# Optimization experiments

Measured on AMD Instinct MI355X. Metric: run time of the kernel, lower is better.

The kernel has to match this reference:

```python
import jax, jax.numpy as jnp
import numpy as np

B, Q, S, D, H = 8, 100, 4096, 256, 8
HD = D // H
EPS = 1e-5


def layer_norm(x, g, b):
    mu = jnp.mean(x, axis=-1, keepdims=True)
    var = jnp.mean(jnp.square(x - mu), axis=-1, keepdims=True)
    return (x - mu) * jax.lax.rsqrt(var + EPS) * g + b


def mha(q_in, k_in, v_in, w_in, b_in, w_out, b_out, bias=None):
    # torch nn.MultiheadAttention math (batch_first, dropout=0)
    wq, wk, wv = jnp.split(w_in, 3, axis=0)
    bq, bk, bv = jnp.split(b_in, 3, axis=0)
    Bq, Lq, _ = q_in.shape
    Lk = k_in.shape[1]
    q = (q_in @ wq.T + bq).reshape(Bq, Lq, H, HD)
    k = (k_in @ wk.T + bk).reshape(Bq, Lk, H, HD)
    v = (v_in @ wv.T + bv).reshape(Bq, Lk, H, HD)
    scores = jnp.einsum('bqhd,bkhd->bhqk', q, k) / jnp.sqrt(jnp.asarray(HD, q.dtype))
    if bias is not None:
        scores = scores + bias  # [B,1,Q,S] broadcast over heads (same per head)
    attn = jax.nn.softmax(scores, axis=-1)
    out = jnp.einsum('bhqk,bkhd->bqhd', attn, v).reshape(Bq, Lq, D)
    return out @ w_out.T + b_out


def setup_inputs() -> dict:
    key = jax.random.key(0)
    ks = jax.random.split(key, 12)
    s = 0.02
    return {
        'queries': jax.random.normal(ks[0], (B, Q, D), jnp.float32),
        'pixel_feat': jax.random.normal(ks[1], (B, S, D), jnp.float32),
        'prev_mask': jax.random.normal(ks[2], (B, Q, S), jnp.float32),
        'cross_in_w': jax.random.normal(ks[3], (3 * D, D), jnp.float32) * s,
        'cross_in_b': jnp.zeros((3 * D,), jnp.float32),
        'cross_out_w': jax.random.normal(ks[4], (D, D), jnp.float32) * s,
        'cross_out_b': jnp.zeros((D,), jnp.float32),
        'self_in_w': jax.random.normal(ks[5], (3 * D, D), jnp.float32) * s,
        'self_in_b': jnp.zeros((3 * D,), jnp.float32),
        'self_out_w': jax.random.normal(ks[6], (D, D), jnp.float32) * s,
        'self_out_b': jnp.zeros((D,), jnp.float32),
        'ln_cross_g': jnp.ones((D,), jnp.float32),
        'ln_cross_b': jnp.zeros((D,), jnp.float32),
        'ln_self_g': jnp.ones((D,), jnp.float32),
        'ln_self_b': jnp.zeros((D,), jnp.float32),
        'ln_ffn_g': jnp.ones((D,), jnp.float32),
        'ln_ffn_b': jnp.zeros((D,), jnp.float32),
        'ffn_w1': jax.random.normal(ks[7], (4 * D, D), jnp.float32) * s,
        'ffn_b1': jnp.zeros((4 * D,), jnp.float32),
        'ffn_w2': jax.random.normal(ks[8], (D, 4 * D), jnp.float32) * s,
        'ffn_b2': jnp.zeros((D,), jnp.float32),
    }


def reference(queries, pixel_feat, prev_mask,
              cross_in_w, cross_in_b, cross_out_w, cross_out_b,
              self_in_w, self_in_b, self_out_w, self_out_b,
              ln_cross_g, ln_cross_b, ln_self_g, ln_self_b, ln_ffn_g, ln_ffn_b,
              ffn_w1, ffn_b1, ffn_w2, ffn_b2):
    # masked cross-attn bias (no-grad region in torch; boolean ops have no grad)
    region = jax.nn.sigmoid(prev_mask) > 0.5                    # [B,Q,S]
    any_pos = jnp.any(region, axis=-1, keepdims=True)
    region = jnp.where(any_pos, region, jnp.ones_like(region))
    bias = (~region).astype(queries.dtype) * -10000.0
    bias = bias[:, None, :, :]                                  # [B,1,Q,S]

    q_out = mha(layer_norm(queries, ln_cross_g, ln_cross_b), pixel_feat, pixel_feat,
                cross_in_w, cross_in_b, cross_out_w, cross_out_b, bias)
    queries = queries + q_out

    q_norm = layer_norm(queries, ln_self_g, ln_self_b)
    q_out = mha(q_norm, q_norm, q_norm, self_in_w, self_in_b, self_out_w, self_out_b)
    queries = queries + q_out

    h = layer_norm(queries, ln_ffn_g, ln_ffn_b)
    h = jax.nn.gelu(h @ ffn_w1.T + ffn_b1, approximate=False) @ ffn_w2.T + ffn_b2
    return queries + h
```

## Files before the change

### kernel.cpp

```cpp
#include <hip/hip_runtime.h>
#include <hip/hip_bf16.h>
#include <math.h>

#define BQ 100
#define SB 8
#define SS 4096
#define DD 256
#define HH 8
#define HDD 32
#define NSPLIT 4
#define SCHUNK (SS / NSPLIT)
#define MROWS 800

typedef __attribute__((ext_vector_type(8))) short bf16x8;
typedef __attribute__((ext_vector_type(4))) float f32x4;

__device__ inline unsigned short f2bf(float f) {
    union { float f; unsigned u; } v; v.f = f;
    unsigned r = v.u + 0x7fff + ((v.u >> 16) & 1);
    return (unsigned short)(r >> 16);
}

__device__ inline unsigned pkbf(float x, float y) {
    union { __hip_bfloat162 h; unsigned u; } c;
    c.h = __float22bfloat162_rn(make_float2(x, y));
    return c.u;
}

__device__ inline bf16x8 load_bf8(const float* p) {
    float4 a = *(const float4*)p;
    float4 b = *(const float4*)(p + 4);
    union { unsigned u[4]; bf16x8 v; } r;
    r.u[0] = pkbf(a.x, a.y); r.u[1] = pkbf(a.z, a.w);
    r.u[2] = pkbf(b.x, b.y); r.u[3] = pkbf(b.z, b.w);
    return r.v;
}

typedef __attribute__((address_space(1))) const void gas_void;
typedef __attribute__((address_space(3))) void las_void;
__device__ inline void gl_lds16(const unsigned short* g, unsigned short* l) {
    __builtin_amdgcn_global_load_lds((gas_void*)g, (las_void*)l, 16, 0, 0);
}

#define TM 128
#define TN 128

#define WOFF_CW   0
#define WOFF_SIW  196608
#define WOFF_COW  393216
#define WOFF_SOW  458752
#define WOFF_F1   524288
#define WOFF_F2   786432
#define WTOT      1048576

__global__ __launch_bounds__(256) void wprep(
        const float* __restrict__ cw, const float* __restrict__ siw,
        const float* __restrict__ cow, const float* __restrict__ sow,
        const float* __restrict__ f1, const float* __restrict__ f2,
        const float* __restrict__ pix,
        unsigned short* __restrict__ o, unsigned short* __restrict__ abf) {
    int b = blockIdx.x;
    int t = threadIdx.x;
    if (b >= 512) {
        size_t off = (size_t)(b - 512) * 2048 + (size_t)t * 8;
        const float* p = pix + off;
        float4 a = *(const float4*)p;
        float4 c = *(const float4*)(p + 4);
        uint4 pk;
        pk.x = pkbf(a.x, a.y); pk.y = pkbf(a.z, a.w);
        pk.z = pkbf(c.x, c.y); pk.w = pkbf(c.z, c.w);
        *(uint4*)(abf + off) = pk;
        return;
    }
    const float* src; size_t so, doff;
    if (b < 96)       { src = cw;  so = (size_t)b * 2048;         doff = WOFF_CW; }
    else if (b < 192) { src = siw; so = (size_t)(b - 96) * 2048;  doff = WOFF_SIW; }
    else if (b < 224) { src = cow; so = (size_t)(b - 192) * 2048; doff = WOFF_COW; }
    else if (b < 256) { src = sow; so = (size_t)(b - 224) * 2048; doff = WOFF_SOW; }
    else if (b < 384) { src = f1;  so = (size_t)(b - 256) * 2048; doff = WOFF_F1; }
    else              { src = f2;  so = (size_t)(b - 384) * 2048; doff = WOFF_F2; }
    const float* p = src + so + (size_t)t * 8;
    float4 a = *(const float4*)p;
    float4 c = *(const float4*)(p + 4);
    uint4 pk;
    pk.x = pkbf(a.x, a.y); pk.y = pkbf(a.z, a.w);
    pk.z = pkbf(c.x, c.y); pk.w = pkbf(c.z, c.w);
    *(uint4*)(o + doff + so + (size_t)t * 8) = pk;
}

__global__ __launch_bounds__(256, 3) void stage1(
        const float* __restrict__ queries,
        const float* __restrict__ ln_g, const float* __restrict__ ln_b,
        const unsigned short* __restrict__ wbf,
        const float* __restrict__ cb,
        float* __restrict__ q_cross,
        const unsigned short* __restrict__ Abf,
        unsigned short* __restrict__ Kb, unsigned short* __restrict__ Vb,
        const float* __restrict__ mask, unsigned* __restrict__ Mbits) {
    __shared__ __align__(16) char smem[32768];
    const int bid = blockIdx.x;
    const int t = threadIdx.x;

    if (bid < 1024) {
        unsigned short* As = (unsigned short*)smem;
        unsigned short* Bs = As + 128 * 64;
        const unsigned short* Wb = wbf + (size_t)DD * DD;
        const float* bias = cb + DD;
        int xcd = bid & 7, idx = bid >> 3;
        int mt = xcd + 8 * (idx >> 2);
        int ntl = idx & 3;
        int m0 = mt * TM, n0 = ntl * TN;
        int wave = t >> 6, lane = t & 63;
        int wm = (wave & 1) * 64, wn = (wave >> 1) * 64;
        int fr = lane & 15, quad = lane >> 4;
        f32x4 acc[4][4] = {};

        int crow[4], ccol[4];
#pragma unroll
        for (int i = 0; i < 4; i++) {
            int c = i * 256 + t;
            crow[i] = c >> 3;
            ccol[i] = (c & 7) ^ (crow[i] & 7);
        }

        for (int k0 = 0; k0 < DD; k0 += 64) {
            __syncthreads();
#pragma unroll
            for (int i = 0; i < 4; i++) {
                gl_lds16(Abf + (size_t)(m0 + crow[i]) * DD + k0 + ccol[i] * 8,
                         As + (i * 256 + t) * 8);
                gl_lds16(Wb + (size_t)(n0 + crow[i]) * DD + k0 + ccol[i] * 8,
                         Bs + (i * 256 + t) * 8);
            }
            __syncthreads();
#pragma unroll
            for (int kk = 0; kk < 2; kk++) {
                bf16x8 af[4], bv[4];
#pragma unroll
                for (int mi = 0; mi < 4; mi++) {
                    int row = wm + mi * 16 + fr;
                    int j = (kk * 4 + quad) ^ (row & 7);
                    af[mi] = *(const bf16x8*)(As + row * 64 + j * 8);
                }
#pragma unroll
                for (int ni = 0; ni < 4; ni++) {
                    int row = wn + ni * 16 + fr;
                    int j = (kk * 4 + quad) ^ (row & 7);
                    bv[ni] = *(const bf16x8*)(Bs + row * 64 + j * 8);
                }
#pragma unroll
                for (int mi = 0; mi < 4; mi++) {
                    acc[mi][0] = __builtin_amdgcn_mfma_f32_16x16x32_bf16(af[mi], bv[0], acc[mi][0], 0, 0, 0);
                    acc[mi][1] = __builtin_amdgcn_mfma_f32_16x16x32_bf16(af[mi], bv[1], acc[mi][1], 0, 0, 0);
                    acc[mi][2] = __builtin_amdgcn_mfma_f32_16x16x32_bf16(af[mi], bv[2], acc[mi][2], 0, 0, 0);
                    acc[mi][3] = __builtin_amdgcn_mfma_f32_16x16x32_bf16(af[mi], bv[3], acc[mi][3], 0, 0, 0);
                }
            }
        }
#pragma unroll
        for (int ni = 0; ni < 4; ni++) {
            int n = n0 + wn + ni * 16 + fr;
            float bv = bias[n];
            unsigned short* dst = (n < 256) ? Kb : Vb;
            int hh = (n >> 5) & 7, d = n & 31;
#pragma unroll
            for (int mi = 0; mi < 4; mi++) {
#pragma unroll
                for (int r = 0; r < 4; r++) {
                    int m = m0 + wm + mi * 16 + quad * 4 + r;
                    int bb = m >> 12, s = m & (SS - 1);
                    dst[((((size_t)bb * HH + hh) * SS + s) << 5) + d] =
                        f2bf(acc[mi][ni][r] + bv);
                }
            }
        }
    } else if (bid < 1824) {
        int row = bid - 1024;
        unsigned* words = (unsigned*)smem;
        unsigned* orred = (unsigned*)(smem + 512);
        int w = t >> 6, lane = t & 63;
        const float* mp = mask + (size_t)row * SS + lane;
        float mv[16];
#pragma unroll
        for (int i = 0; i < 16; i++) mv[i] = mp[(w * 16 + i) * 64];
        unsigned lor = 0;
#pragma unroll
        for (int i = 0; i < 16; i++) {
            unsigned long long bal = __ballot(mv[i] > 0.f);
            if (lane == 0) {
                words[(w * 16 + i) * 2] = (unsigned)bal;
                words[(w * 16 + i) * 2 + 1] = (unsigned)(bal >> 32);
            }
            lor |= (unsigned)(bal | (bal >> 32));
        }
        if (lane == 0) orred[w] = lor;
        __syncthreads();
        unsigned anyv = orred[0] | orred[1] | orred[2] | orred[3];
        if (t < 128) Mbits[(size_t)row * 128 + t] = anyv ? words[t] : 0xFFFFFFFFu;
    } else {
        typedef unsigned short (*arow_t)[264];
        arow_t Aq = (arow_t)smem;
        float* mu_s = (float*)(smem + 16896);
        float* rs_s = mu_s + 32;
        float (*prt)[8][2] = (float(*)[8][2])(rs_s + 32);
        int idx = bid - 1824;
        int nq = idx & 1, my = idx >> 1;
        int m0 = my * 32;
        int row = t & 31, cs = t >> 5;
        const float* xp = queries + (size_t)(m0 + row) * DD + cs * 32;
        float s = 0.f, ss = 0.f;
#pragma unroll
        for (int c = 0; c < 32; c += 4) {
            float4 v = *(const float4*)(xp + c);
            s += v.x + v.y + v.z + v.w;
            ss += v.x * v.x + v.y * v.y + v.z * v.z + v.w * v.w;
        }
        prt[row][cs][0] = s; prt[row][cs][1] = ss;
        __syncthreads();
        if (t < 32) {
            float sum = 0.f, sq = 0.f;
#pragma unroll
            for (int k = 0; k < 8; k++) { sum += prt[t][k][0]; sq += prt[t][k][1]; }
            float mu = sum * (1.0f / DD);
            float var = sq * (1.0f / DD) - mu * mu;
            mu_s[t] = mu;
            rs_s[t] = rsqrtf(var + 1e-5f);
        }
        __syncthreads();
        {
            float mu = mu_s[row], r = rs_s[row];
            int col0 = cs * 32;
#pragma unroll
            for (int c = 0; c < 32; c += 8) {
                int col = col0 + c;
                float4 v0 = *(const float4*)(xp + c);
                float4 v1 = *(const float4*)(xp + c + 4);
                float4 g0 = *(const float4*)(ln_g + col);
                float4 g1 = *(const float4*)(ln_g + col + 4);
                float4 b0 = *(const float4*)(ln_b + col);
                float4 b1 = *(const float4*)(ln_b + col + 4);
                uint4 pk;
                pk.x = pkbf((v0.x - mu) * r * g0.x + b0.x, (v0.y - mu) * r * g0.y + b0.y);
                pk.y = pkbf((v0.z - mu) * r * g0.z + b0.z, (v0.w - mu) * r * g0.w + b0.w);
                pk.z = pkbf((v1.x - mu) * r * g1.x + b1.x, (v1.y - mu) * r * g1.y + b1.y);
                pk.w = pkbf((v1.z - mu) * r * g1.z + b1.z, (v1.w - mu) * r * g1.w + b1.w);
                *(uint4*)&Aq[row][col] = pk;
            }
        }
        __syncthreads();
        int w = t >> 6, lane = t & 63;
        int fr = lane & 15, quad = lane >> 4;
        int n0 = nq * 128 + w * 32;
        f32x4 acc[2][2] = {};
        const unsigned short* Wq0 = wbf + (size_t)(n0 + fr) * DD + quad * 8;
        const unsigned short* Wq1 = Wq0 + (size_t)16 * DD;
#pragma unroll
        for (int k0 = 0; k0 < DD; k0 += 32) {
            bf16x8 a0 = *(const bf16x8*)&Aq[fr][k0 + quad * 8];
            bf16x8 a1 = *(const bf16x8*)&Aq[16 + fr][k0 + quad * 8];
            bf16x8 w0 = *(const bf16x8*)(Wq0 + k0);
            bf16x8 w1 = *(const bf16x8*)(Wq1 + k0);
            acc[0][0] = __builtin_amdgcn_mfma_f32_16x16x32_bf16(a0, w0, acc[0][0], 0, 0, 0);
            acc[0][1] = __builtin_amdgcn_mfma_f32_16x16x32_bf16(a0, w1, acc[0][1], 0, 0, 0);
            acc[1][0] = __builtin_amdgcn_mfma_f32_16x16x32_bf16(a1, w0, acc[1][0], 0, 0, 0);
            acc[1][1] = __builtin_amdgcn_mfma_f32_16x16x32_bf16(a1, w1, acc[1][1], 0, 0, 0);
        }
#pragma unroll
        for (int ni = 0; ni < 2; ni++) {
            int n = n0 + ni * 16 + fr;
            float bv = cb[n];
#pragma unroll
            for (int mi = 0; mi < 2; mi++) {
#pragma unroll
                for (int r = 0; r < 4; r++) {
                    int m = m0 + mi * 16 + quad * 4 + r;
                    q_cross[(size_t)m * DD + n] = acc[mi][ni][r] + bv;
                }
            }
        }
    }
}

template<int MODE>
__global__ __launch_bounds__(64, 4) void ln_gemm(
        const float* __restrict__ X, const float* __restrict__ gam,
        const float* __restrict__ bet,
        const unsigned short* __restrict__ W, const float* __restrict__ bias,
        const float* __restrict__ res,
        float* __restrict__ C, int N) {
    __shared__ unsigned short As[32][264];
    __shared__ float mu_s[32], rs_s[32];
    __shared__ float prt[32][2][2];
    const int t = threadIdx.x;
    const int fr = t & 15, quad = t >> 4;
    const int m0 = blockIdx.y * 32, n0 = blockIdx.x * 32;
    const int row = t & 31, half = t >> 5;

    const float* xp = X + (size_t)(m0 + row) * DD + half * 128;
    float s = 0.f, ss = 0.f;
#pragma unroll
    for (int c = 0; c < 128; c += 4) {
        float4 v = *(const float4*)(xp + c);
        s += v.x + v.y + v.z + v.w;
        ss += v.x * v.x + v.y * v.y + v.z * v.z + v.w * v.w;
    }
    prt[row][half][0] = s;
    prt[row][half][1] = ss;
    __syncthreads();
    if (t < 32) {
        float sum = prt[t][0][0] + prt[t][1][0];
        float sq  = prt[t][0][1] + prt[t][1][1];
        float mu = sum * (1.0f / DD);
        float var = sq * (1.0f / DD) - mu * mu;
        mu_s[t] = mu;
        rs_s[t] = rsqrtf(var + 1e-5f);
    }
    __syncthreads();
    {
        float mu = mu_s[row], r = rs_s[row];
#pragma unroll
        for (int c = 0; c < 128; c += 8) {
            int col = half * 128 + c;
            float4 v0 = *(const float4*)(xp + c);
            float4 v1 = *(const float4*)(xp + c + 4);
            float4 g0 = *(const float4*)(gam + col);
            float4 g1 = *(const float4*)(gam + col + 4);
            float4 b0 = *(const float4*)(bet + col);
            float4 b1 = *(const float4*)(bet + col + 4);
            uint4 pk;
            pk.x = pkbf((v0.x - mu) * r * g0.x + b0.x, (v0.y - mu) * r * g0.y + b0.y);
            pk.y = pkbf((v0.z - mu) * r * g0.z + b0.z, (v0.w - mu) * r * g0.w + b0.w);
            pk.z = pkbf((v1.x - mu) * r * g1.x + b1.x, (v1.y - mu) * r * g1.y + b1.y);
            pk.w = pkbf((v1.z - mu) * r * g1.z + b1.z, (v1.w - mu) * r * g1.w + b1.w);
            *(uint4*)&As[row][col] = pk;
        }
    }
    __syncthreads();

    f32x4 acc[2][2] = {};
    const unsigned short* Wp0 = W + (size_t)(n0 + fr) * DD + quad * 8;
    const unsigned short* Wp1 = Wp0 + (size_t)16 * DD;
#pragma unroll
    for (int k0 = 0; k0 < DD; k0 += 32) {
        bf16x8 a0 = *(const bf16x8*)&As[fr][k0 + quad * 8];
        bf16x8 a1 = *(const bf16x8*)&As[16 + fr][k0 + quad * 8];
        bf16x8 w0 = *(const bf16x8*)(Wp0 + k0);
        bf16x8 w1 = *(const bf16x8*)(Wp1 + k0);
        acc[0][0] = __builtin_amdgcn_mfma_f32_16x16x32_bf16(a0, w0, acc[0][0], 0, 0, 0);
        acc[0][1] = __builtin_amdgcn_mfma_f32_16x16x32_bf16(a0, w1, acc[0][1], 0, 0, 0);
        acc[1][0] = __builtin_amdgcn_mfma_f32_16x16x32_bf16(a1, w0, acc[1][0], 0, 0, 0);
        acc[1][1] = __builtin_amdgcn_mfma_f32_16x16x32_bf16(a1, w1, acc[1][1], 0, 0, 0);
    }

#pragma unroll
    for (int ni = 0; ni < 2; ni++) {
        int n = n0 + ni * 16 + fr;
        float bv = bias[n];
#pragma unroll
        for (int mi = 0; mi < 2; mi++) {
#pragma unroll
            for (int r = 0; r < 4; r++) {
                int m = m0 + mi * 16 + quad * 4 + r;
                float v = acc[mi][ni][r] + bv;
                if (MODE == 1) {
                    v = 0.5f * v * (1.0f + erff(v * 0.70710678118654752f));
                } else if (MODE == 2) {
                    v += res[(size_t)m * N + n];
                }
                C[(size_t)m * N + n] = v;
            }
        }
    }
}

__global__ __launch_bounds__(64, 4) void comb_gemm(
        const float* __restrict__ Opart, const float* __restrict__ mpart,
        const float* __restrict__ lpart,
        const unsigned short* __restrict__ W, const float* __restrict__ bias,
        const float* __restrict__ res,
        float* __restrict__ C) {
    __shared__ unsigned short As[32][264];
    const int t = threadIdx.x;
    const int fr = t & 15, quad = t >> 4;
    const int m0 = blockIdx.y * 32, n0 = blockIdx.x * 32;
    const int row = t & 31, half = t >> 5;

    {
        int m = m0 + row;
        int b = m / BQ, q = m % BQ;
#pragma unroll
        for (int h = half * 4; h < half * 4 + 4; h++) {
            float mv[NSPLIT], wsp[NSPLIT];
            float mstar = -1e30f;
#pragma unroll
            for (int sp = 0; sp < NSPLIT; sp++) {
                mv[sp] = mpart[((size_t)(b * NSPLIT + sp) * HH + h) * BQ + q];
                mstar = fmaxf(mstar, mv[sp]);
            }
            float lstar = 0.f;
#pragma unroll
            for (int sp = 0; sp < NSPLIT; sp++) {
                wsp[sp] = __expf(mv[sp] - mstar);
                lstar += lpart[((size_t)(b * NSPLIT + sp) * HH + h) * BQ + q] * wsp[sp];
            }
            float inv = 1.0f / lstar;
#pragma unroll
            for (int d = 0; d < HDD; d += 8) {
                float o[8] = {};
#pragma unroll
                for (int sp = 0; sp < NSPLIT; sp++) {
                    const float* op = Opart +
                        ((size_t)(b * NSPLIT + sp) * BQ + q) * DD + h * HDD + d;
                    float4 a = *(const float4*)op;
                    float4 b4 = *(const float4*)(op + 4);
                    o[0] += a.x * wsp[sp];  o[1] += a.y * wsp[sp];
                    o[2] += a.z * wsp[sp];  o[3] += a.w * wsp[sp];
                    o[4] += b4.x * wsp[sp]; o[5] += b4.y * wsp[sp];
                    o[6] += b4.z * wsp[sp]; o[7] += b4.w * wsp[sp];
                }
                uint4 pk;
                pk.x = pkbf(o[0] * inv, o[1] * inv);
                pk.y = pkbf(o[2] * inv, o[3] * inv);
                pk.z = pkbf(o[4] * inv, o[5] * inv);
                pk.w = pkbf(o[6] * inv, o[7] * inv);
                *(uint4*)&As[row][h * HDD + d] = pk;
            }
        }
    }
    __syncthreads();

    f32x4 acc[2][2] = {};
    const unsigned short* Wp0 = W + (size_t)(n0 + fr) * DD + quad * 8;
    const unsigned short* Wp1 = Wp0 + (size_t)16 * DD;
#pragma unroll
    for (int k0 = 0; k0 < DD; k0 += 32) {
        bf16x8 a0 = *(const bf16x8*)&As[fr][k0 + quad * 8];
        bf16x8 a1 = *(const bf16x8*)&As[16 + fr][k0 + quad * 8];
        bf16x8 w0 = *(const bf16x8*)(Wp0 + k0);
        bf16x8 w1 = *(const bf16x8*)(Wp1 + k0);
        acc[0][0] = __builtin_amdgcn_mfma_f32_16x16x32_bf16(a0, w0, acc[0][0], 0, 0, 0);
        acc[0][1] = __builtin_amdgcn_mfma_f32_16x16x32_bf16(a0, w1, acc[0][1], 0, 0, 0);
        acc[1][0] = __builtin_amdgcn_mfma_f32_16x16x32_bf16(a1, w0, acc[1][0], 0, 0, 0);
        acc[1][1] = __builtin_amdgcn_mfma_f32_16x16x32_bf16(a1, w1, acc[1][1], 0, 0, 0);
    }

#pragma unroll
    for (int ni = 0; ni < 2; ni++) {
        int n = n0 + ni * 16 + fr;
        float bv = bias[n];
#pragma unroll
        for (int mi = 0; mi < 2; mi++) {
#pragma unroll
            for (int r = 0; r < 4; r++) {
                int m = m0 + mi * 16 + quad * 4 + r;
                float v = acc[mi][ni][r] + bv + res[(size_t)m * DD + n];
                C[(size_t)m * DD + n] = v;
            }
        }
    }
}

template<int KK, int SPLITK, int MODE>
__global__ __launch_bounds__(64, 4) void gemm_skinny2(
        const float* __restrict__ A, const unsigned short* __restrict__ W,
        const float* __restrict__ bias, const float* __restrict__ res,
        float* __restrict__ C, float* __restrict__ Cp, int N) {
    const int lane = threadIdx.x;
    const int fr = lane & 15, quad = lane >> 4;
    const int m0 = blockIdx.y * 32;
    const int n0 = blockIdx.x * 32;
    const int sk = blockIdx.z;
    const int KCH = KK / SPLITK;

    f32x4 acc[2][2] = {};
    const float* Ap0 = A + (size_t)(m0 + fr) * KK + sk * KCH + quad * 8;
    const float* Ap1 = Ap0 + (size_t)16 * KK;
    const unsigned short* Wp0 = W + (size_t)(n0 + fr) * KK + sk * KCH + quad * 8;
    const unsigned short* Wp1 = Wp0 + (size_t)16 * KK;

#pragma unroll
    for (int k0 = 0; k0 < KCH; k0 += 32) {
        bf16x8 a0 = load_bf8(Ap0 + k0);
        bf16x8 a1 = load_bf8(Ap1 + k0);
        bf16x8 w0 = *(const bf16x8*)(Wp0 + k0);
        bf16x8 w1 = *(const bf16x8*)(Wp1 + k0);
        acc[0][0] = __builtin_amdgcn_mfma_f32_16x16x32_bf16(a0, w0, acc[0][0], 0, 0, 0);
        acc[0][1] = __builtin_amdgcn_mfma_f32_16x16x32_bf16(a0, w1, acc[0][1], 0, 0, 0);
        acc[1][0] = __builtin_amdgcn_mfma_f32_16x16x32_bf16(a1, w0, acc[1][0], 0, 0, 0);
        acc[1][1] = __builtin_amdgcn_mfma_f32_16x16x32_bf16(a1, w1, acc[1][1], 0, 0, 0);
    }

    if (SPLITK == 1) {
#pragma unroll
        for (int ni = 0; ni < 2; ni++) {
            int n = n0 + ni * 16 + fr;
            float bv = bias[n];
#pragma unroll
            for (int mi = 0; mi < 2; mi++) {
#pragma unroll
                for (int r = 0; r < 4; r++) {
                    int m = m0 + mi * 16 + quad * 4 + r;
                    float v = acc[mi][ni][r] + bv;
                    if (MODE == 1) {
                        v = 0.5f * v * (1.0f + erff(v * 0.70710678118654752f));
                    } else if (MODE == 2) {
                        v += res[(size_t)m * N + n];
                    }
                    C[(size_t)m * N + n] = v;
                }
            }
        }
    } else {
        float* dst = Cp + (size_t)sk * MROWS * N;
#pragma unroll
        for (int ni = 0; ni < 2; ni++) {
            int n = n0 + ni * 16 + fr;
#pragma unroll
            for (int mi = 0; mi < 2; mi++) {
#pragma unroll
                for (int r = 0; r < 4; r++) {
                    int m = m0 + mi * 16 + quad * 4 + r;
                    dst[(size_t)m * N + n] = acc[mi][ni][r];
                }
            }
        }
    }
}

template<int SPLITK, int MODE>
__global__ void gemm_combine(const float* __restrict__ Cp,
                             const float* __restrict__ bias,
                             const float* __restrict__ res,
                             float* __restrict__ C, int N) {
    int m = blockIdx.x;
    for (int n = threadIdx.x; n < N; n += 256) {
        float v = bias[n];
#pragma unroll
        for (int sk = 0; sk < SPLITK; sk++)
            v += Cp[((size_t)sk * MROWS + m) * N + n];
        if (MODE == 1) {
            v = 0.5f * v * (1.0f + erff(v * 0.70710678118654752f));
        } else if (MODE == 2) {
            v += res[(size_t)m * N + n];
        }
        C[(size_t)m * N + n] = v;
    }
}

#define QT 64
#define ST 128

__global__ __launch_bounds__(256) void cross_attn_mfma(
        const float* __restrict__ Qm,
        const unsigned short* __restrict__ Kb,
        const unsigned short* __restrict__ Vb,
        const unsigned* __restrict__ Mbits,
        float* __restrict__ Opart,
        float* __restrict__ mpart,
        float* __restrict__ lpart) {
    __shared__ unsigned short Qs[QT][40];
    __shared__ unsigned short Ks[ST][40];
    __shared__ unsigned short Vt[HDD][136];
    __shared__ unsigned short Ps[QT][136];
    __shared__ unsigned Mq[QT][4];
    __shared__ float red[QT][17];
    __shared__ float m_s[QT], alpha_s[QT], l_s[QT];

    const int qb = blockIdx.x, h = blockIdx.y;
    const int b = blockIdx.z / NSPLIT, sp = blockIdx.z % NSPLIT;
    const int t = threadIdx.x;
    const int w = t >> 6, lane = t & 63;
    const int fr = lane & 15, quad = lane >> 4;
    const int q0 = qb * QT;
    const int qlim = min(BQ - q0, QT);

    {
        int q = t >> 2, c0 = (t & 3) * 8;
        float4 v0 = make_float4(0.f, 0.f, 0.f, 0.f), v1 = v0;
        if (q < qlim) {
            const float* qp = Qm + (size_t)(b * BQ + q0 + q) * DD + h * HDD + c0;
            v0 = *(const float4*)qp;
            v1 = *(const float4*)(qp + 4);
        }
        const float sc = 0.17677669529663687f;
        uint4 pq;
        pq.x = pkbf(v0.x * sc, v0.y * sc);
        pq.y = pkbf(v0.z * sc, v0.w * sc);
        pq.z = pkbf(v1.x * sc, v1.y * sc);
        pq.w = pkbf(v1.z * sc, v1.w * sc);
        *(uint4*)&Qs[q][c0] = pq;
        if (t < QT) { m_s[t] = -1e30f; l_s[t] = 0.f; }
    }

    f32x4 oacc[2] = {};
    const unsigned short* Kbase = Kb + (((size_t)(b * HH + h)) * SS << 5);
    const unsigned short* Vbase = Vb + (((size_t)(b * HH + h)) * SS << 5);

    for (int s0 = sp * SCHUNK; s0 < (sp + 1) * SCHUNK; s0 += ST) {
        __syncthreads();
        {
            int r = t >> 1, half = t & 1;
            const unsigned short* kp = Kbase + ((size_t)(s0 + r) << 5) + half * 16;
            *(uint4*)&Ks[r][half * 16] = *(const uint4*)kp;
            *(uint4*)&Ks[r][half * 16 + 8] = *(const uint4*)(kp + 8);
            const unsigned short* vp = Vbase + ((size_t)(s0 + r) << 5) + half * 16;
            union { uint4 u; unsigned short s[8]; } v0, v1;
            v0.u = *(const uint4*)vp;
            v1.u = *(const uint4*)(vp + 8);
#pragma unroll
            for (int j = 0; j < 8; j++) Vt[half * 16 + j][r] = v0.s[j];
#pragma unroll
            for (int j = 0; j < 8; j++) Vt[half * 16 + 8 + j][r] = v1.s[j];
        }
        {
            int q = t >> 2, wd = t & 3;
            unsigned mword = 0xFFFFFFFFu;
            if (q < qlim)
                mword = Mbits[(size_t)(b * BQ + q0 + q) * 128 + (s0 >> 5) + wd];
            Mq[q][wd] = mword;
        }
        __syncthreads();

        bf16x8 af[2];
#pragma unroll
        for (int mt = 0; mt < 2; mt++)
            af[mt] = *(const bf16x8*)&Ks[w * 32 + mt * 16 + fr][quad * 8];
        f32x4 st[2][4];
#pragma unroll
        for (int nt = 0; nt < 4; nt++) {
            bf16x8 bq = *(const bf16x8*)&Qs[nt * 16 + fr][quad * 8];
#pragma unroll
            for (int mt = 0; mt < 2; mt++) {
                f32x4 z = {0.f, 0.f, 0.f, 0.f};
                st[mt][nt] = __builtin_amdgcn_mfma_f32_16x16x32_bf16(af[mt], bq, z, 0, 0, 0);
            }
        }

        float pmax[4] = {-1e30f, -1e30f, -1e30f, -1e30f};
#pragma unroll
        for (int nt = 0; nt < 4; nt++) {
            unsigned mword = Mq[nt * 16 + fr][w];
#pragma unroll
            for (int mt = 0; mt < 2; mt++)
#pragma unroll
                for (int r = 0; r < 4; r++) {
                    int bitpos = mt * 16 + quad * 4 + r;
                    float v = st[mt][nt][r];
                    if (!((mword >> bitpos) & 1u)) v -= 10000.f;
                    st[mt][nt][r] = v;
                    pmax[nt] = fmaxf(pmax[nt], v);
                }
        }
#pragma unroll
        for (int nt = 0; nt < 4; nt++)
            red[nt * 16 + fr][w * 4 + quad] = pmax[nt];
        __syncthreads();

        if (t < QT) {
            float mt_ = -1e30f;
#pragma unroll
            for (int k = 0; k < 16; k++) mt_ = fmaxf(mt_, red[t][k]);
            float mo = m_s[t], mn = fmaxf(mo, mt_);
            m_s[t] = mn;
            alpha_s[t] = __expf(mo - mn);
        }
        __syncthreads();

        float psum[4] = {0.f, 0.f, 0.f, 0.f};
#pragma unroll
        for (int nt = 0; nt < 4; nt++) {
            float mrow = m_s[nt * 16 + fr];
#pragma unroll
            for (int mt = 0; mt < 2; mt++) {
                float p0 = __expf(st[mt][nt][0] - mrow);
                float p1 = __expf(st[mt][nt][1] - mrow);
                float p2 = __expf(st[mt][nt][2] - mrow);
                float p3 = __expf(st[mt][nt][3] - mrow);
                psum[nt] += p0 + p1 + p2 + p3;
                uint2 pk;
                pk.x = pkbf(p0, p1);
                pk.y = pkbf(p2, p3);
                *(uint2*)&Ps[nt * 16 + fr][w * 32 + mt * 16 + quad * 4] = pk;
            }
        }
#pragma unroll
        for (int nt = 0; nt < 4; nt++)
            red[nt * 16 + fr][w * 4 + quad] = psum[nt];
        __syncthreads();

        if (t < QT) {
            float s = 0.f;
#pragma unroll
            for (int k = 0; k < 16; k++) s += red[t][k];
            l_s[t] = l_s[t] * alpha_s[t] + s;
        }

#pragma unroll
        for (int r = 0; r < 4; r++) {
            float a = alpha_s[w * 16 + quad * 4 + r];
            oacc[0][r] *= a; oacc[1][r] *= a;
        }
#pragma unroll
        for (int k0 = 0; k0 < ST; k0 += 32) {
            bf16x8 ap = *(const bf16x8*)&Ps[w * 16 + fr][k0 + quad * 8];
            bf16x8 bv0 = *(const bf16x8*)&Vt[fr][k0 + quad * 8];
            bf16x8 bv1 = *(const bf16x8*)&Vt[16 + fr][k0 + quad * 8];
            oacc[0] = __builtin_amdgcn_mfma_f32_16x16x32_bf16(ap, bv0, oacc[0], 0, 0, 0);
            oacc[1] = __builtin_amdgcn_mfma_f32_16x16x32_bf16(ap, bv1, oacc[1], 0, 0, 0);
        }
    }
    __syncthreads();

    int part = b * NSPLIT + sp;
    if (t < qlim) {
        mpart[((size_t)part * HH + h) * BQ + q0 + t] = m_s[t];
        lpart[((size_t)part * HH + h) * BQ + q0 + t] = l_s[t];
    }
#pragma unroll
    for (int nd = 0; nd < 2; nd++) {
#pragma unroll
        for (int r = 0; r < 4; r++) {
            int q = w * 16 + quad * 4 + r;
            if (q < qlim)
                Opart[((size_t)part * BQ + q0 + q) * DD + h * HDD + nd * 16 + fr] = oacc[nd][r];
        }
    }
}

__global__ void attn_kernel(const float* __restrict__ Qm, int sq, int qo0,
                            const float* __restrict__ Km, int sk, int ko0,
                            const float* __restrict__ Vm, int sv, int vo0,
                            float* __restrict__ Out, int so, int oo0,
                            int Slen, int Qlen, float scale) {
    int q = blockIdx.x, h = blockIdx.y, b = blockIdx.z;
    int tid = threadIdx.x;
    __shared__ float qv[32];
    __shared__ float sc[128];
    __shared__ float red[256];
    __shared__ float part[8][33];
    int qrow = b * Qlen + q;
    if (tid < 32) qv[tid] = Qm[(size_t)qrow * sq + qo0 + h * HDD + tid] * scale;
    __syncthreads();

    float lmax = -1e30f;
    for (int s = tid; s < Slen; s += 256) {
        const float* kp = Km + (size_t)(b * Slen + s) * sk + ko0 + h * HDD;
        float dot = 0.f;
#pragma unroll
        for (int d = 0; d < HDD; d += 4) {
            float4 k4 = *(const float4*)(kp + d);
            dot += qv[d] * k4.x + qv[d + 1] * k4.y + qv[d + 2] * k4.z + qv[d + 3] * k4.w;
        }
        sc[s] = dot;
        lmax = fmaxf(lmax, dot);
    }
    red[tid] = lmax; __syncthreads();
    for (int off = 128; off > 0; off >>= 1) {
        if (tid < off) red[tid] = fmaxf(red[tid], red[tid + off]);
        __syncthreads();
    }
    float m = red[0];
    __syncthreads();
    float lsum = 0.f;
    for (int s = tid; s < Slen; s += 256) {
        float e = __expf(sc[s] - m);
        sc[s] = e;
        lsum += e;
    }
    red[tid] = lsum; __syncthreads();
    for (int off = 128; off > 0; off >>= 1) {
        if (tid < off) red[tid] += red[tid + off];
        __syncthreads();
    }
    float inv = 1.0f / red[0];

    int d = tid & 31, g = tid >> 5;
    float acc = 0.f;
    for (int s = g; s < Slen; s += 8)
        acc += sc[s] * Vm[(size_t)(b * Slen + s) * sv + vo0 + h * HDD + d];
    part[g][d] = acc; __syncthreads();
    if (g == 0) {
        float t = 0.f;
#pragma unroll
        for (int gg = 0; gg < 8; gg++) t += part[gg][d];
        Out[(size_t)qrow * so + oo0 + h * HDD + d] = t * inv;
    }
}

extern "C" void kernel_launch(void* const* d_in, const int* in_sizes, int n_in,
                              void* d_out, int out_size, void* d_ws, size_t ws_size,
                              hipStream_t stream) {
    const float* queries    = (const float*)d_in[0];
    const float* pixel_feat = (const float*)d_in[1];
    const float* prev_mask  = (const float*)d_in[2];
    const float* cross_in_w  = (const float*)d_in[3];
    const float* cross_in_b  = (const float*)d_in[4];
    const float* cross_out_w = (const float*)d_in[5];
    const float* cross_out_b = (const float*)d_in[6];
    const float* self_in_w   = (const float*)d_in[7];
    const float* self_in_b   = (const float*)d_in[8];
    const float* self_out_w  = (const float*)d_in[9];
    const float* self_out_b  = (const float*)d_in[10];
    const float* ln_cross_g  = (const float*)d_in[11];
    const float* ln_cross_b  = (const float*)d_in[12];
    const float* ln_self_g   = (const float*)d_in[13];
    const float* ln_self_b   = (const float*)d_in[14];
    const float* ln_ffn_g    = (const float*)d_in[15];
    const float* ln_ffn_b    = (const float*)d_in[16];
    const float* ffn_w1 = (const float*)d_in[17];
    const float* ffn_b1 = (const float*)d_in[18];
    const float* ffn_w2 = (const float*)d_in[19];
    const float* ffn_b2 = (const float*)d_in[20];
    float* out = (float*)d_out;

    const int NQ = SB * BQ;
    const int NK = SB * SS;

    float* ws = (float*)d_ws;
    unsigned* Mbits = (unsigned*)ws;   ws += (size_t)NQ * 128;
    float* q_cross  = ws;              ws += (size_t)NQ * DD;
    unsigned short* Kbk = (unsigned short*)ws;
    ws += (size_t)NK * DD / 2;
    unsigned short* Vbk = (unsigned short*)ws;
    ws += (size_t)NK * DD / 2;
    float* queries1 = ws;              ws += (size_t)NQ * DD;
    float* qkv      = ws;              ws += (size_t)NQ * 3 * DD;
    float* attn2    = ws;              ws += (size_t)NQ * DD;
    float* queries2 = ws;              ws += (size_t)NQ * DD;
    float* ffn_h    = ws;              ws += (size_t)NQ * 4 * DD;
    float* Csplit   = ws;              ws += (size_t)4 * MROWS * DD;
    float* Opart    = ws;              ws += (size_t)SB * NSPLIT * BQ * DD;
    float* mpart    = ws;              ws += (size_t)SB * NSPLIT * HH * BQ;
    float* lpart    = ws;              ws += (size_t)SB * NSPLIT * HH * BQ;
    unsigned short* wbf = (unsigned short*)ws;
    ws += WTOT / 2;
    unsigned short* Abf = (unsigned short*)ws;

    const float scale = 0.17677669529663687f;

    wprep<<<4608, 256, 0, stream>>>(
        cross_in_w, self_in_w, cross_out_w, self_out_w, ffn_w1, ffn_w2,
        pixel_feat, wbf, Abf);

    stage1<<<1874, 256, 0, stream>>>(
        queries, ln_cross_g, ln_cross_b, wbf, cross_in_b, q_cross,
        Abf, Kbk, Vbk, prev_mask, Mbits);

    cross_attn_mfma<<<dim3(2, HH, SB * NSPLIT), 256, 0, stream>>>(
        q_cross, Kbk, Vbk, Mbits, Opart, mpart, lpart);
    comb_gemm<<<dim3(8, 25), 64, 0, stream>>>(
        Opart, mpart, lpart, wbf + WOFF_COW, cross_out_b, queries, queries1);

    ln_gemm<0><<<dim3(24, 25), 64, 0, stream>>>(
        queries1, ln_self_g, ln_self_b, wbf + WOFF_SIW, self_in_b, nullptr,
        qkv, 3 * DD);
    attn_kernel<<<dim3(BQ, HH, SB), 256, 0, stream>>>(
        qkv, 3 * DD, 0, qkv, 3 * DD, DD, qkv, 3 * DD, 2 * DD,
        attn2, DD, 0, BQ, BQ, scale);
    gemm_skinny2<256, 1, 2><<<dim3(8, 25), 64, 0, stream>>>(
        attn2, wbf + WOFF_SOW, self_out_b, queries1, queries2, nullptr, DD);

    ln_gemm<1><<<dim3(32, 25), 64, 0, stream>>>(
        queries2, ln_ffn_g, ln_ffn_b, wbf + WOFF_F1, ffn_b1, nullptr,
        ffn_h, 4 * DD);
    gemm_skinny2<1024, 4, 2><<<dim3(8, 25, 4), 64, 0, stream>>>(
        ffn_h, wbf + WOFF_F2, ffn_b2, nullptr, nullptr, Csplit, DD);
    gemm_combine<4, 2><<<MROWS, 256, 0, stream>>>(
        Csplit, ffn_b2, queries2, out, DD);
}
```

Measured before the change: 253.9 us.

## Double-buffer K/V projection GEMM and replace scalar self-attention with MFMA kernel

The K/V projection GEMM in stage1 now uses a 32-wide K step with two LDS buffers. The next tile's loads are issued before computing on the current one, so a single barrier per step replaces the previous load/compute barrier pair. Separately, the per-query scalar self-attention kernel (800 blocks) is replaced by one block per (head, batch) that computes scores, softmax and P·V with bf16 MFMA. This drops scalar FP32 dot products and many small reductions, but lowers self-attention precision to bf16 and uses far fewer blocks.

```diff
diff --git a/kernel.cpp b/kernel.cpp
--- a/kernel.cpp
+++ b/kernel.cpp
@@ -102,60 +102,63 @@
     const int t = threadIdx.x;
 
     if (bid < 1024) {
-        unsigned short* As = (unsigned short*)smem;
-        unsigned short* Bs = As + 128 * 64;
+        unsigned short* Sbuf = (unsigned short*)smem;
         const unsigned short* Wb = wbf + (size_t)DD * DD;
         const float* bias = cb + DD;
         int xcd = bid & 7, idx = bid >> 3;
-        int mt = xcd + 8 * (idx >> 2);
+        int mtile = xcd + 8 * (idx >> 2);
         int ntl = idx & 3;
-        int m0 = mt * TM, n0 = ntl * TN;
+        int m0 = mtile * TM, n0 = ntl * TN;
         int wave = t >> 6, lane = t & 63;
         int wm = (wave & 1) * 64, wn = (wave >> 1) * 64;
         int fr = lane & 15, quad = lane >> 4;
         f32x4 acc[4][4] = {};
 
-        int crow[4], ccol[4];
-#pragma unroll
-        for (int i = 0; i < 4; i++) {
-            int c = i * 256 + t;
-            crow[i] = c >> 3;
-            ccol[i] = (c & 7) ^ (crow[i] & 7);
-        }
-
-        for (int k0 = 0; k0 < DD; k0 += 64) {
+        const int c0 = t, c1 = 256 + t;
+        const int r0 = c0 >> 2, r1 = c1 >> 2;
+        const int cc0 = (c0 & 3) ^ ((r0 >> 1) & 3);
+        const int cc1 = (c1 & 3) ^ ((r1 >> 1) & 3);
+
+        gl_lds16(Abf + (size_t)(m0 + r0) * DD + cc0 * 8, Sbuf + c0 * 8);
+        gl_lds16(Abf + (size_t)(m0 + r1) * DD + cc1 * 8, Sbuf + c1 * 8);
+        gl_lds16(Wb + (size_t)(n0 + r0) * DD + cc0 * 8, Sbuf + 4096 + c0 * 8);
+        gl_lds16(Wb + (size_t)(n0 + r1) * DD + cc1 * 8, Sbuf + 4096 + c1 * 8);
+        __syncthreads();
+
+#pragma unroll
+        for (int ks = 0; ks < 8; ks++) {
+            unsigned short* Ab = Sbuf + (ks & 1) * 8192;
+            unsigned short* Bb = Ab + 4096;
+            if (ks < 7) {
+                unsigned short* An = Sbuf + ((ks + 1) & 1) * 8192;
+                unsigned short* Bn = An + 4096;
+                int k0 = (ks + 1) * 32;
+                gl_lds16(Abf + (size_t)(m0 + r0) * DD + k0 + cc0 * 8, An + c0 * 8);
+                gl_lds16(Abf + (size_t)(m0 + r1) * DD + k0 + cc1 * 8, An + c1 * 8);
+                gl_lds16(Wb + (size_t)(n0 + r0) * DD + k0 + cc0 * 8, Bn + c0 * 8);
+                gl_lds16(Wb + (size_t)(n0 + r1) * DD + k0 + cc1 * 8, Bn + c1 * 8);
+            }
+            bf16x8 af[4], bv[4];
+#pragma unroll
+            for (int mi = 0; mi < 4; mi++) {
+                int row = wm + mi * 16 + fr;
+                int j = quad ^ ((row >> 1) & 3);
+                af[mi] = *(const bf16x8*)(Ab + row * 32 + j * 8);
+            }
+#pragma unroll
+            for (int ni = 0; ni < 4; ni++) {
+                int row = wn + ni * 16 + fr;
+                int j = quad ^ ((row >> 1) & 3);
+                bv[ni] = *(const bf16x8*)(Bb + row * 32 + j * 8);
+            }
+#pragma unroll
+            for (int mi = 0; mi < 4; mi++) {
+                acc[mi][0] = __builtin_amdgcn_mfma_f32_16x16x32_bf16(af[mi], bv[0], acc[mi][0], 0, 0, 0);
+                acc[mi][1] = __builtin_amdgcn_mfma_f32_16x16x32_bf16(af[mi], bv[1], acc[mi][1], 0, 0, 0);
+                acc[mi][2] = __builtin_amdgcn_mfma_f32_16x16x32_bf16(af[mi], bv[2], acc[mi][2], 0, 0, 0);
+                acc[mi][3] = __builtin_amdgcn_mfma_f32_16x16x32_bf16(af[mi], bv[3], acc[mi][3], 0, 0, 0);
+            }
             __syncthreads();
-#pragma unroll
-            for (int i = 0; i < 4; i++) {
-                gl_lds16(Abf + (size_t)(m0 + crow[i]) * DD + k0 + ccol[i] * 8,
-                         As + (i * 256 + t) * 8);
-                gl_lds16(Wb + (size_t)(n0 + crow[i]) * DD + k0 + ccol[i] * 8,
-                         Bs + (i * 256 + t) * 8);
-            }
-            __syncthreads();
-#pragma unroll
-            for (int kk = 0; kk < 2; kk++) {
-                bf16x8 af[4], bv[4];
-#pragma unroll
-                for (int mi = 0; mi < 4; mi++) {
-                    int row = wm + mi * 16 + fr;
-                    int j = (kk * 4 + quad) ^ (row & 7);
-                    af[mi] = *(const bf16x8*)(As + row * 64 + j * 8);
-                }
-#pragma unroll
-                for (int ni = 0; ni < 4; ni++) {
-                    int row = wn + ni * 16 + fr;
-                    int j = (kk * 4 + quad) ^ (row & 7);
-                    bv[ni] = *(const bf16x8*)(Bs + row * 64 + j * 8);
-                }
-#pragma unroll
-                for (int mi = 0; mi < 4; mi++) {
-                    acc[mi][0] = __builtin_amdgcn_mfma_f32_16x16x32_bf16(af[mi], bv[0], acc[mi][0], 0, 0, 0);
-                    acc[mi][1] = __builtin_amdgcn_mfma_f32_16x16x32_bf16(af[mi], bv[1], acc[mi][1], 0, 0, 0);
-                    acc[mi][2] = __builtin_amdgcn_mfma_f32_16x16x32_bf16(af[mi], bv[2], acc[mi][2], 0, 0, 0);
-                    acc[mi][3] = __builtin_amdgcn_mfma_f32_16x16x32_bf16(af[mi], bv[3], acc[mi][3], 0, 0, 0);
-                }
-            }
         }
 #pragma unroll
         for (int ni = 0; ni < 4; ni++) {
@@ -727,63 +730,151 @@
     }
 }
 
-__global__ void attn_kernel(const float* __restrict__ Qm, int sq, int qo0,
-                            const float* __restrict__ Km, int sk, int ko0,
-                            const float* __restrict__ Vm, int sv, int vo0,
-                            float* __restrict__ Out, int so, int oo0,
-                            int Slen, int Qlen, float scale) {
-    int q = blockIdx.x, h = blockIdx.y, b = blockIdx.z;
-    int tid = threadIdx.x;
-    __shared__ float qv[32];
-    __shared__ float sc[128];
-    __shared__ float red[256];
-    __shared__ float part[8][33];
-    int qrow = b * Qlen + q;
-    if (tid < 32) qv[tid] = Qm[(size_t)qrow * sq + qo0 + h * HDD + tid] * scale;
+__global__ __launch_bounds__(256) void self_attn_mfma(
+        const float* __restrict__ qkv, float* __restrict__ Out) {
+    __shared__ unsigned short Qs[128][40];
+    __shared__ unsigned short Vt[HDD][136];
+    __shared__ unsigned short Ps[112][136];
+    __shared__ float red[112][17];
+    __shared__ float m_s[112], l_s[112];
+
+    const int h = blockIdx.x, b = blockIdx.y;
+    const int t = threadIdx.x;
+    const int w = t >> 6, lane = t & 63;
+    const int fr = lane & 15, quad = lane >> 4;
+    const float sc = 0.17677669529663687f;
+
+    {
+        int r = t >> 1, half = t & 1;
+        float4 a0 = make_float4(0.f, 0.f, 0.f, 0.f), a1 = a0, a2 = a0, a3 = a0;
+        float4 c0 = a0, c1 = a0, c2 = a0, c3 = a0;
+        if (r < BQ) {
+            const float* qp = qkv + (size_t)(b * BQ + r) * 768 + h * HDD + half * 16;
+            a0 = *(const float4*)qp;       a1 = *(const float4*)(qp + 4);
+            a2 = *(const float4*)(qp + 8); a3 = *(const float4*)(qp + 12);
+            const float* vp = qp + 512;
+            c0 = *(const float4*)vp;       c1 = *(const float4*)(vp + 4);
+            c2 = *(const float4*)(vp + 8); c3 = *(const float4*)(vp + 12);
+        }
+        uint4 p0, p1;
+        p0.x = pkbf(a0.x * sc, a0.y * sc); p0.y = pkbf(a0.z * sc, a0.w * sc);
+        p0.z = pkbf(a1.x * sc, a1.y * sc); p0.w = pkbf(a1.z * sc, a1.w * sc);
+        p1.x = pkbf(a2.x * sc, a2.y * sc); p1.y = pkbf(a2.z * sc, a2.w * sc);
+        p1.z = pkbf(a3.x * sc, a3.y * sc); p1.w = pkbf(a3.z * sc, a3.w * sc);
+        *(uint4*)&Qs[r][half * 16] = p0;
+        *(uint4*)&Qs[r][half * 16 + 8] = p1;
+        float vv[16] = {c0.x, c0.y, c0.z, c0.w, c1.x, c1.y, c1.z, c1.w,
+                        c2.x, c2.y, c2.z, c2.w, c3.x, c3.y, c3.z, c3.w};
+#pragma unroll
+        for (int j = 0; j < 16; j++) Vt[half * 16 + j][r] = f2bf(vv[j]);
+    }
     __syncthreads();
 
-    float lmax = -1e30f;
-    for (int s = tid; s < Slen; s += 256) {
-        const float* kp = Km + (size_t)(b * Slen + s) * sk + ko0 + h * HDD;
-        float dot = 0.f;
-#pragma unroll
-        for (int d = 0; d < HDD; d += 4) {
-            float4 k4 = *(const float4*)(kp + d);
-            dot += qv[d] * k4.x + qv[d + 1] * k4.y + qv[d + 2] * k4.z + qv[d + 3] * k4.w;
-        }
-        sc[s] = dot;
-        lmax = fmaxf(lmax, dot);
-    }
-    red[tid] = lmax; __syncthreads();
-    for (int off = 128; off > 0; off >>= 1) {
-        if (tid < off) red[tid] = fmaxf(red[tid], red[tid + off]);
-        __syncthreads();
-    }
-    float m = red[0];
+    bf16x8 af[2];
+#pragma unroll
+    for (int mt = 0; mt < 2; mt++) {
+        int s = w * 32 + mt * 16 + fr;
+        bf16x8 kz = {0, 0, 0, 0, 0, 0, 0, 0};
+        af[mt] = kz;
+        if (s < BQ)
+            af[mt] = load_bf8(qkv + (size_t)(b * BQ + s) * 768 + 256 + h * HDD + quad * 8);
+    }
+    f32x4 st[2][7];
+#pragma unroll
+    for (int nt = 0; nt < 7; nt++) {
+        bf16x8 bq = *(const bf16x8*)&Qs[nt * 16 + fr][quad * 8];
+#pragma unroll
+        for (int mt = 0; mt < 2; mt++) {
+            f32x4 z = {0.f, 0.f, 0.f, 0.f};
+            st[mt][nt] = __builtin_amdgcn_mfma_f32_16x16x32_bf16(af[mt], bq, z, 0, 0, 0);
+        }
+    }
+
+    float pmax[7];
+#pragma unroll
+    for (int nt = 0; nt < 7; nt++) {
+        pmax[nt] = -1e30f;
+#pragma unroll
+        for (int mt = 0; mt < 2; mt++)
+#pragma unroll
+            for (int r = 0; r < 4; r++) {
+                int s = w * 32 + mt * 16 + quad * 4 + r;
+                float v = st[mt][nt][r];
+                if (s >= BQ) v = -1e30f;
+                st[mt][nt][r] = v;
+                pmax[nt] = fmaxf(pmax[nt], v);
+            }
+        red[nt * 16 + fr][w * 4 + quad] = pmax[nt];
+    }
     __syncthreads();
-    float lsum = 0.f;
-    for (int s = tid; s < Slen; s += 256) {
-        float e = __expf(sc[s] - m);
-        sc[s] = e;
-        lsum += e;
-    }
-    red[tid] = lsum; __syncthreads();
-    for (int off = 128; off > 0; off >>= 1) {
-        if (tid < off) red[tid] += red[tid + off];
-        __syncthreads();
-    }
-    float inv = 1.0f / red[0];
-
-    int d = tid & 31, g = tid >> 5;
-    float acc = 0.f;
-    for (int s = g; s < Slen; s += 8)
-        acc += sc[s] * Vm[(size_t)(b * Slen + s) * sv + vo0 + h * HDD + d];
-    part[g][d] = acc; __syncthreads();
-    if (g == 0) {
-        float t = 0.f;
-#pragma unroll
-        for (int gg = 0; gg < 8; gg++) t += part[gg][d];
-        Out[(size_t)qrow * so + oo0 + h * HDD + d] = t * inv;
+    if (t < 112) {
+        float m = -1e30f;
+#pragma unroll
+        for (int k = 0; k < 16; k++) m = fmaxf(m, red[t][k]);
+        m_s[t] = m;
+    }
+    __syncthreads();
+
+    float psum[7];
+#pragma unroll
+    for (int nt = 0; nt < 7; nt++) {
+        float mrow = m_s[nt * 16 + fr];
+        psum[nt] = 0.f;
+#pragma unroll
+        for (int mt = 0; mt < 2; mt++) {
+            float p0 = __expf(st[mt][nt][0] - mrow);
+            float p1 = __expf(st[mt][nt][1] - mrow);
+            float p2 = __expf(st[mt][nt][2] - mrow);
+            float p3 = __expf(st[mt][nt][3] - mrow);
+            psum[nt] += p0 + p1 + p2 + p3;
+            uint2 pk;
+            pk.x = pkbf(p0, p1);
+            pk.y = pkbf(p2, p3);
+            *(uint2*)&Ps[nt * 16 + fr][w * 32 + mt * 16 + quad * 4] = pk;
+        }
+        red[nt * 16 + fr][w * 4 + quad] = psum[nt];
+    }
+    __syncthreads();
+    if (t < 112) {
+        float s = 0.f;
+#pragma unroll
+        for (int k = 0; k < 16; k++) s += red[t][k];
+        l_s[t] = s;
+    }
+    __syncthreads();
+
+    f32x4 oacc[2][2] = {};
+#pragma unroll
+    for (int ti = 0; ti < 2; ti++) {
+        int qt = w + ti * 4;
+        if (qt < 7) {
+#pragma unroll
+            for (int k0 = 0; k0 < 128; k0 += 32) {
+                bf16x8 ap = *(const bf16x8*)&Ps[qt * 16 + fr][k0 + quad * 8];
+                bf16x8 bv0 = *(const bf16x8*)&Vt[fr][k0 + quad * 8];
+                bf16x8 bv1 = *(const bf16x8*)&Vt[16 + fr][k0 + quad * 8];
+                oacc[ti][0] = __builtin_amdgcn_mfma_f32_16x16x32_bf16(ap, bv0, oacc[ti][0], 0, 0, 0);
+                oacc[ti][1] = __builtin_amdgcn_mfma_f32_16x16x32_bf16(ap, bv1, oacc[ti][1], 0, 0, 0);
+            }
+        }
+    }
+#pragma unroll
+    for (int ti = 0; ti < 2; ti++) {
+        int qt = w + ti * 4;
+        if (qt < 7) {
+#pragma unroll
+            for (int nd = 0; nd < 2; nd++) {
+#pragma unroll
+                for (int r = 0; r < 4; r++) {
+                    int q = qt * 16 + quad * 4 + r;
+                    if (q < BQ) {
+                        float inv = 1.0f / l_s[q];
+                        Out[(size_t)(b * BQ + q) * DD + h * HDD + nd * 16 + fr] =
+                            oacc[ti][nd][r] * inv;
+                    }
+                }
+            }
+        }
     }
 }
 
@@ -837,6 +928,7 @@
     unsigned short* Abf = (unsigned short*)ws;
 
     const float scale = 0.17677669529663687f;
+    (void)scale;
 
     wprep<<<4608, 256, 0, stream>>>(
         cross_in_w, self_in_w, cross_out_w, self_out_w, ffn_w1, ffn_w2,
@@ -854,9 +946,7 @@
     ln_gemm<0><<<dim3(24, 25), 64, 0, stream>>>(
         queries1, ln_self_g, ln_self_b, wbf + WOFF_SIW, self_in_b, nullptr,
         qkv, 3 * DD);
-    attn_kernel<<<dim3(BQ, HH, SB), 256, 0, stream>>>(
-        qkv, 3 * DD, 0, qkv, 3 * DD, DD, qkv, 3 * DD, 2 * DD,
-        attn2, DD, 0, BQ, BQ, scale);
+    self_attn_mfma<<<dim3(HH, SB), 256, 0, stream>>>(qkv, attn2);
     gemm_skinny2<256, 1, 2><<<dim3(8, 25), 64, 0, stream>>>(
         attn2, wbf + WOFF_SOW, self_out_b, queries1, queries2, nullptr, DD);
 
```

New measurement: 230.7 us. -9.1%, faster.
